# Performance work log

Measured on AMD Instinct MI355X. Metric: run time of the kernel, lower is better.

Reference implementation:

```python
import jax, jax.numpy as jnp
import numpy as np

N_NODES = 100000
N_EDGES = 3200000
IN_DIM = 128


def setup_inputs() -> dict:
    key = jax.random.key(0)
    ks = jax.random.split(key, 6)
    x = jax.random.normal(ks[0], (N_NODES, IN_DIM), dtype=jnp.float32)
    edge_index = jax.random.randint(ks[1], (2, N_EDGES), 0, N_NODES, dtype=jnp.int64)
    # Glorot-ish init for weights, zero bias (PyG GCNConv default has bias)
    W1 = jax.random.normal(ks[2], (IN_DIM, 32), dtype=jnp.float32) / np.sqrt(IN_DIM)
    b1 = jnp.zeros((32,), dtype=jnp.float32)
    W2 = jax.random.normal(ks[3], (32, 16), dtype=jnp.float32) / np.sqrt(32.0)
    b2 = jnp.zeros((16,), dtype=jnp.float32)
    Wf = jax.random.normal(ks[4], (16, 1), dtype=jnp.float32) / np.sqrt(16.0)
    bf = jnp.zeros((1,), dtype=jnp.float32)
    return {"x": x, "edge_index": edge_index, "W1": W1, "b1": b1,
            "W2": W2, "b2": b2, "Wf": Wf, "bf": bf}


def reference(x, edge_index, W1, b1, W2, b2, Wf, bf):
    N = x.shape[0]
    # PyG GCNConv: add self-loops, symmetric normalization D^-1/2 (A+I) D^-1/2
    loop = jnp.arange(N, dtype=edge_index.dtype)
    src = jnp.concatenate([edge_index[0], loop])  # message sources (x_j)
    dst = jnp.concatenate([edge_index[1], loop])  # aggregation targets
    deg = jax.ops.segment_sum(jnp.ones_like(dst, dtype=x.dtype), dst, num_segments=N)
    dinv = jax.lax.rsqrt(jnp.maximum(deg, 1.0))  # deg >= 1 due to self-loops
    norm = dinv[src] * dinv[dst]                  # per-edge coefficient

    def gcn_conv(h, W, b):
        h = h @ W                                 # linear transform first (small dim)
        msg = h[src] * norm[:, None]              # gather + scale
        return jax.ops.segment_sum(msg, dst, num_segments=N) + b  # scatter-add

    h = jax.nn.relu(gcn_conv(x, W1, b1))
    h = jax.nn.relu(gcn_conv(h, W2, b2))
    return (h @ Wf + bf).squeeze(-1)              # [N]
```

## Files before the change

kernel.cpp:

```cpp
#include <hip/hip_runtime.h>


#define TPB 256
#define NBUCK 512
#define BCAP 8192
#define CHUNK 8192

__device__ __forceinline__ unsigned f2bf(float f) {
    unsigned u = __float_as_uint(f);
    return (u + 0x7FFFu + ((u >> 16) & 1u)) >> 16;
}
__device__ __forceinline__ float bflo(unsigned u) { return __uint_as_float(u << 16); }
__device__ __forceinline__ float bfhi(unsigned u) { return __uint_as_float(u & 0xFFFF0000u); }

__global__ __launch_bounds__(512) void binA2_kernel(
        const int* __restrict__ src, const int* __restrict__ dst,
        int* __restrict__ bcur, unsigned* __restrict__ staging, int E, int NPB) {
    __shared__ unsigned packed[CHUNK];
    __shared__ unsigned short buckb[CHUNK];
    __shared__ int hist[NBUCK];
    __shared__ int scan_[NBUCK];
    __shared__ int lstart[NBUCK];
    __shared__ int lcur[NBUCK];
    __shared__ int gbase[NBUCK];
    int tid = threadIdx.x;
    int start = blockIdx.x * CHUNK;
    int sz = min(CHUNK, E - start);

    hist[tid] = 0;
    __syncthreads();
    for (int i = tid; i < sz; i += 512) {
        unsigned d = (unsigned)dst[start + i];
        atomicAdd(&hist[d / (unsigned)NPB], 1);
    }
    __syncthreads();
    int v = hist[tid];
    scan_[tid] = v;
    __syncthreads();
    for (int dd = 1; dd < NBUCK; dd <<= 1) {
        int t = (tid >= dd) ? scan_[tid - dd] : 0;
        __syncthreads();
        scan_[tid] += t;
        __syncthreads();
    }
    lstart[tid] = scan_[tid] - v;
    lcur[tid] = 0;
    gbase[tid] = atomicAdd(&bcur[tid], v);
    __syncthreads();
    for (int i = tid; i < sz; i += 512) {
        unsigned d = (unsigned)dst[start + i];
        unsigned s = (unsigned)src[start + i];
        unsigned b = d / (unsigned)NPB;
        unsigned loc = d - b * (unsigned)NPB;
        int pos = atomicAdd(&lcur[b], 1);
        int si = lstart[b] + pos;
        packed[si] = (loc << 20) | s;
        buckb[si] = (unsigned short)b;
    }
    __syncthreads();
    for (int i = tid; i < sz; i += 512) {
        unsigned b = buckb[i];
        int dsti = gbase[b] + (i - lstart[b]);
        if (dsti < BCAP)
            staging[(size_t)b * BCAP + dsti] = packed[i];
    }
}

__global__ void buildB_kernel(const int* __restrict__ bcur,
                              const unsigned* __restrict__ staging,
                              int* __restrict__ offs, int* __restrict__ counts,
                              float* __restrict__ dinv, int* __restrict__ csr_src,
                              int N, int NPB) {
    __shared__ int sb[NBUCK];
    __shared__ int hist[512];
    __shared__ int scan_[512];
    __shared__ int cur[512];
    int b = blockIdx.x;
    int tid = threadIdx.x;
    if (tid < NBUCK) sb[tid] = min(bcur[tid], BCAP);
    __syncthreads();
    for (int d = 1; d < NBUCK; d <<= 1) {
        int t = 0;
        if (tid < NBUCK && tid >= d) t = sb[tid - d];
        __syncthreads();
        if (tid < NBUCK) sb[tid] += t;
        __syncthreads();
    }
    int sz = min(bcur[b], BCAP);
    int base = (b == 0) ? 0 : sb[b - 1];
    int n0 = b * NPB;
    int nn = min(NPB, N - n0);
    const unsigned* se = staging + (size_t)b * BCAP;

    hist[tid] = 0;
    __syncthreads();
    for (int i = tid; i < sz; i += 512)
        atomicAdd(&hist[se[i] >> 20], 1);
    __syncthreads();
    int h = hist[tid];
    scan_[tid] = h;
    __syncthreads();
    for (int d = 1; d < 512; d <<= 1) {
        int t = (tid >= d) ? scan_[tid - d] : 0;
        __syncthreads();
        scan_[tid] += t;
        __syncthreads();
    }
    int excl = scan_[tid] - h;
    cur[tid] = excl;
    if (tid < nn) {
        int node = n0 + tid;
        offs[node] = base + excl;
        counts[node] = h;
        dinv[node] = rsqrtf((float)(h + 1));
    }
    __syncthreads();
    for (int i = tid; i < sz; i += 512) {
        unsigned p = se[i];
        int pos = atomicAdd(&cur[p >> 20], 1);
        csr_src[base + pos] = (int)(p & 0xFFFFFu);
    }
}

__global__ __launch_bounds__(256) void gemm1_kernel(
        const float* __restrict__ x, const float* __restrict__ W1,
        const float* __restrict__ dinv, unsigned* __restrict__ xwd, int N) {
    __shared__ float ws_[128 * 32];
    for (int i = threadIdx.x; i < 128 * 32; i += 256) ws_[i] = W1[i];
    __syncthreads();
    int t = threadIdx.x;
    int jq = (t & 3) * 8;
    int n0 = blockIdx.x * 256 + (t >> 2) * 4;
    if (n0 >= N) return;
    int nc0 = min(n0 + 0, N - 1);
    int nc1 = min(n0 + 1, N - 1);
    int nc2 = min(n0 + 2, N - 1);
    int nc3 = min(n0 + 3, N - 1);
    const float4* xr0 = (const float4*)(x + (size_t)nc0 * 128);
    const float4* xr1 = (const float4*)(x + (size_t)nc1 * 128);
    const float4* xr2 = (const float4*)(x + (size_t)nc2 * 128);
    const float4* xr3 = (const float4*)(x + (size_t)nc3 * 128);
    float acc[4][8];
#pragma unroll
    for (int n = 0; n < 4; ++n)
#pragma unroll
        for (int j = 0; j < 8; ++j) acc[n][j] = 0.0f;
#pragma unroll 2
    for (int k4 = 0; k4 < 32; ++k4) {
        const float* wb = ws_ + (k4 * 4) * 32 + jq;
        float4 a0 = *(const float4*)(wb);
        float4 a1 = *(const float4*)(wb + 4);
        float4 b0 = *(const float4*)(wb + 32);
        float4 b1v = *(const float4*)(wb + 36);
        float4 c0 = *(const float4*)(wb + 64);
        float4 c1 = *(const float4*)(wb + 68);
        float4 d0 = *(const float4*)(wb + 96);
        float4 d1 = *(const float4*)(wb + 100);
        float4 xv0 = xr0[k4];
        float4 xv1 = xr1[k4];
        float4 xv2 = xr2[k4];
        float4 xv3 = xr3[k4];
#pragma unroll
        for (int n = 0; n < 4; ++n) {
            float4 xv = (n == 0) ? xv0 : (n == 1) ? xv1 : (n == 2) ? xv2 : xv3;
            acc[n][0] += xv.x * a0.x + xv.y * b0.x + xv.z * c0.x + xv.w * d0.x;
            acc[n][1] += xv.x * a0.y + xv.y * b0.y + xv.z * c0.y + xv.w * d0.y;
            acc[n][2] += xv.x * a0.z + xv.y * b0.z + xv.z * c0.z + xv.w * d0.z;
            acc[n][3] += xv.x * a0.w + xv.y * b0.w + xv.z * c0.w + xv.w * d0.w;
            acc[n][4] += xv.x * a1.x + xv.y * b1v.x + xv.z * c1.x + xv.w * d1.x;
            acc[n][5] += xv.x * a1.y + xv.y * b1v.y + xv.z * c1.y + xv.w * d1.y;
            acc[n][6] += xv.x * a1.z + xv.y * b1v.z + xv.z * c1.z + xv.w * d1.z;
            acc[n][7] += xv.x * a1.w + xv.y * b1v.w + xv.z * c1.w + xv.w * d1.w;
        }
    }
#pragma unroll
    for (int n = 0; n < 4; ++n) {
        int node = n0 + n;
        if (node >= N) break;
        float d = dinv[node];
        unsigned pk0 = f2bf(acc[n][0] * d) | (f2bf(acc[n][1] * d) << 16);
        unsigned pk1 = f2bf(acc[n][2] * d) | (f2bf(acc[n][3] * d) << 16);
        unsigned pk2 = f2bf(acc[n][4] * d) | (f2bf(acc[n][5] * d) << 16);
        unsigned pk3 = f2bf(acc[n][6] * d) | (f2bf(acc[n][7] * d) << 16);
        ((uint4*)(xwd + (size_t)node * 16))[t & 3] = make_uint4(pk0, pk1, pk2, pk3);
    }
}

__global__ __launch_bounds__(256) void aggF_kernel(
        const int* __restrict__ offs, const int* __restrict__ counts,
        const int* __restrict__ csr_src, const float* __restrict__ dinv,
        const unsigned* __restrict__ xwd, const float* __restrict__ b1,
        const float* __restrict__ W2, unsigned* __restrict__ h2wd, int N) {
    __shared__ float ws2[32 * 16];
    for (int i = threadIdx.x; i < 512; i += 256) ws2[i] = W2[i];
    __syncthreads();
    int t = threadIdx.x;
    int q = t & 3;
    int node = blockIdx.x * 64 + (t >> 2);
    if (node >= N) return;
    int off = offs[node];
    int deg = counts[node];
    float acc[8];
    {
        uint4 v = ((const uint4*)(xwd + (size_t)node * 16))[q];
        acc[0] = bflo(v.x); acc[1] = bfhi(v.x);
        acc[2] = bflo(v.y); acc[3] = bfhi(v.y);
        acc[4] = bflo(v.z); acc[5] = bfhi(v.z);
        acc[6] = bflo(v.w); acc[7] = bfhi(v.w);
    }
    int i = 0;
    for (; i + 3 < deg; i += 4) {
        int s0 = csr_src[off + i];
        int s1 = csr_src[off + i + 1];
        int s2 = csr_src[off + i + 2];
        int s3 = csr_src[off + i + 3];
        uint4 v0 = ((const uint4*)(xwd + (size_t)s0 * 16))[q];
        uint4 v1 = ((const uint4*)(xwd + (size_t)s1 * 16))[q];
        uint4 v2 = ((const uint4*)(xwd + (size_t)s2 * 16))[q];
        uint4 v3 = ((const uint4*)(xwd + (size_t)s3 * 16))[q];
        acc[0] += (bflo(v0.x) + bflo(v1.x)) + (bflo(v2.x) + bflo(v3.x));
        acc[1] += (bfhi(v0.x) + bfhi(v1.x)) + (bfhi(v2.x) + bfhi(v3.x));
        acc[2] += (bflo(v0.y) + bflo(v1.y)) + (bflo(v2.y) + bflo(v3.y));
        acc[3] += (bfhi(v0.y) + bfhi(v1.y)) + (bfhi(v2.y) + bfhi(v3.y));
        acc[4] += (bflo(v0.z) + bflo(v1.z)) + (bflo(v2.z) + bflo(v3.z));
        acc[5] += (bfhi(v0.z) + bfhi(v1.z)) + (bfhi(v2.z) + bfhi(v3.z));
        acc[6] += (bflo(v0.w) + bflo(v1.w)) + (bflo(v2.w) + bflo(v3.w));
        acc[7] += (bfhi(v0.w) + bfhi(v1.w)) + (bfhi(v2.w) + bfhi(v3.w));
    }
    for (; i < deg; ++i) {
        int s = csr_src[off + i];
        uint4 v = ((const uint4*)(xwd + (size_t)s * 16))[q];
        acc[0] += bflo(v.x); acc[1] += bfhi(v.x);
        acc[2] += bflo(v.y); acc[3] += bfhi(v.y);
        acc[4] += bflo(v.z); acc[5] += bfhi(v.z);
        acc[6] += bflo(v.w); acc[7] += bfhi(v.w);
    }
    float dv = dinv[node];
    float part[16];
#pragma unroll
    for (int j = 0; j < 16; ++j) part[j] = 0.0f;
    const float* bq = b1 + q * 8;
#pragma unroll
    for (int k = 0; k < 8; ++k) {
        float h = fmaxf(acc[k] * dv + bq[k], 0.0f);
        const float* wr = ws2 + (q * 8 + k) * 16;
        float4 w0 = *(const float4*)(wr);
        float4 w1 = *(const float4*)(wr + 4);
        float4 w2 = *(const float4*)(wr + 8);
        float4 w3 = *(const float4*)(wr + 12);
        part[0]  += h * w0.x; part[1]  += h * w0.y; part[2]  += h * w0.z; part[3]  += h * w0.w;
        part[4]  += h * w1.x; part[5]  += h * w1.y; part[6]  += h * w1.z; part[7]  += h * w1.w;
        part[8]  += h * w2.x; part[9]  += h * w2.y; part[10] += h * w2.z; part[11] += h * w2.w;
        part[12] += h * w3.x; part[13] += h * w3.y; part[14] += h * w3.z; part[15] += h * w3.w;
    }
    float p8[8];
#pragma unroll
    for (int j = 0; j < 8; ++j) {
        float send = (q & 1) ? part[j] : part[j + 8];
        float keep = (q & 1) ? part[j + 8] : part[j];
        p8[j] = keep + __shfl_xor(send, 1, 64);
    }
    float p4[4];
#pragma unroll
    for (int j = 0; j < 4; ++j) {
        float send = (q & 2) ? p8[j] : p8[j + 4];
        float keep = (q & 2) ? p8[j + 4] : p8[j];
        p4[j] = keep + __shfl_xor(send, 2, 64);
    }
    unsigned pk0 = f2bf(p4[0] * dv) | (f2bf(p4[1] * dv) << 16);
    unsigned pk1 = f2bf(p4[2] * dv) | (f2bf(p4[3] * dv) << 16);
    int slot = ((q & 1) << 1) | ((q >> 1) & 1);
    ((uint2*)(h2wd + (size_t)node * 8))[slot] = make_uint2(pk0, pk1);
}

__global__ __launch_bounds__(256) void aggS16f_kernel(
        const int* __restrict__ offs, const int* __restrict__ counts,
        const int* __restrict__ csr_src, const float* __restrict__ dinv,
        const unsigned* __restrict__ h2wd,
        const float* __restrict__ b2, const float* __restrict__ Wf,
        const float* __restrict__ bf, float* __restrict__ out, int N) {
    __shared__ float bs_[16];
    __shared__ float wf_[16];
    __shared__ float bfv;
    int t = threadIdx.x;
    if (t < 16) { bs_[t] = b2[t]; wf_[t] = Wf[t]; }
    if (t == 0) bfv = bf[0];
    __syncthreads();
    int q = t & 1;
    int node = blockIdx.x * 128 + (t >> 1);
    if (node >= N) return;
    int off = offs[node];
    int deg = counts[node];
    float acc[8];
    {
        uint4 v = ((const uint4*)(h2wd + (size_t)node * 8))[q];
        acc[0] = bflo(v.x); acc[1] = bfhi(v.x);
        acc[2] = bflo(v.y); acc[3] = bfhi(v.y);
        acc[4] = bflo(v.z); acc[5] = bfhi(v.z);
        acc[6] = bflo(v.w); acc[7] = bfhi(v.w);
    }
    int i = 0;
    for (; i + 3 < deg; i += 4) {
        int s0 = csr_src[off + i];
        int s1 = csr_src[off + i + 1];
        int s2 = csr_src[off + i + 2];
        int s3 = csr_src[off + i + 3];
        uint4 v0 = ((const uint4*)(h2wd + (size_t)s0 * 8))[q];
        uint4 v1 = ((const uint4*)(h2wd + (size_t)s1 * 8))[q];
        uint4 v2 = ((const uint4*)(h2wd + (size_t)s2 * 8))[q];
        uint4 v3 = ((const uint4*)(h2wd + (size_t)s3 * 8))[q];
        acc[0] += (bflo(v0.x) + bflo(v1.x)) + (bflo(v2.x) + bflo(v3.x));
        acc[1] += (bfhi(v0.x) + bfhi(v1.x)) + (bfhi(v2.x) + bfhi(v3.x));
        acc[2] += (bflo(v0.y) + bflo(v1.y)) + (bflo(v2.y) + bflo(v3.y));
        acc[3] += (bfhi(v0.y) + bfhi(v1.y)) + (bfhi(v2.y) + bfhi(v3.y));
        acc[4] += (bflo(v0.z) + bflo(v1.z)) + (bflo(v2.z) + bflo(v3.z));
        acc[5] += (bfhi(v0.z) + bfhi(v1.z)) + (bfhi(v2.z) + bfhi(v3.z));
        acc[6] += (bflo(v0.w) + bflo(v1.w)) + (bflo(v2.w) + bflo(v3.w));
        acc[7] += (bfhi(v0.w) + bfhi(v1.w)) + (bfhi(v2.w) + bfhi(v3.w));
    }
    for (; i < deg; ++i) {
        int s = csr_src[off + i];
        uint4 v = ((const uint4*)(h2wd + (size_t)s * 8))[q];
        acc[0] += bflo(v.x); acc[1] += bfhi(v.x);
        acc[2] += bflo(v.y); acc[3] += bfhi(v.y);
        acc[4] += bflo(v.z); acc[5] += bfhi(v.z);
        acc[6] += bflo(v.w); acc[7] += bfhi(v.w);
    }
    float dv = dinv[node];
    const float* bq = bs_ + q * 8;
    const float* wq = wf_ + q * 8;
    float part = 0.f;
#pragma unroll
    for (int k = 0; k < 8; ++k)
        part += fmaxf(acc[k] * dv + bq[k], 0.f) * wq[k];
    part += __shfl_xor(part, 1, 64);
    if (q == 0) out[node] = part + bfv;
}

extern "C" void kernel_launch(void* const* d_in, const int* in_sizes, int n_in,
                              void* d_out, int out_size, void* d_ws, size_t ws_size,
                              hipStream_t stream) {
    const float* x  = (const float*)d_in[0];
    const int*   ei = (const int*)d_in[1];
    const float* W1 = (const float*)d_in[2];
    const float* b1 = (const float*)d_in[3];
    const float* W2 = (const float*)d_in[4];
    const float* b2 = (const float*)d_in[5];
    const float* Wf = (const float*)d_in[6];
    const float* bf = (const float*)d_in[7];

    int N = in_sizes[0] / 128;
    int E = in_sizes[1] / 2;
    const int* src = ei;
    const int* dst = ei + E;
    int NPB = (N + NBUCK - 1) / NBUCK;

    size_t Np = ((size_t)N + 3) & ~(size_t)3;
    size_t Ep = ((size_t)E + 3) & ~(size_t)3;
    int* wsI      = (int*)d_ws;
    int* counts   = wsI;
    int* offs     = counts + Np;
    int* bcur     = offs + Np;
    int* csr_src  = bcur + NBUCK;
    float* dinv   = (float*)(csr_src + Ep);
    unsigned* xwd = (unsigned*)(dinv + Np);
    unsigned* staging = xwd + 16 * Np;
    unsigned* h2wd = staging;
    float* out    = (float*)d_out;

    int nbG1 = (N + 255) / 256;
    int nbC  = (E + CHUNK - 1) / CHUNK;
    int nbA32 = (N + 63) / 64;
    int nbA16 = (N + 127) / 128;

    hipMemsetAsync(bcur, 0, NBUCK * sizeof(int), stream);
    binA2_kernel<<<nbC, 512, 0, stream>>>(src, dst, bcur, staging, E, NPB);
    buildB_kernel<<<NBUCK, 512, 0, stream>>>(bcur, staging, offs, counts,
                                             dinv, csr_src, N, NPB);
    gemm1_kernel<<<nbG1, 256, 0, stream>>>(x, W1, dinv, xwd, N);
    aggF_kernel<<<nbA32, 256, 0, stream>>>(offs, counts, csr_src, dinv, xwd,
                                           b1, W2, h2wd, N);
    aggS16f_kernel<<<nbA16, 256, 0, stream>>>(offs, counts, csr_src, dinv, h2wd,
                                              b2, Wf, bf, out, N);
}
```

Before: 253.3 us.

## Use wave-shuffle scans, register-staged binning, split bucket base scan, smaller GEMM tiles

Replaces the shared-memory Hillis-Steele scans with a wave-shuffle exclusive scan, and halves CHUNK so the binning kernel runs more blocks. The binning kernels now keep edge data in registers instead of reading global memory twice. The per-block redundant 512-entry bucket scan in buildB moves into a separate single-block kernel, and gemm1 handles 2 nodes per thread instead of 4 for more blocks. In exchange it adds one kernel launch and raises register pressure; buildB's 16-register staging assumes bucket size stays within BCAP.

```diff
diff --git a/kernel.cpp b/kernel.cpp
--- a/kernel.cpp
+++ b/kernel.cpp
@@ -4,7 +4,7 @@
 #define TPB 256
 #define NBUCK 512
 #define BCAP 8192
-#define CHUNK 8192
+#define CHUNK 4096
 
 __device__ __forceinline__ unsigned f2bf(float f) {
     unsigned u = __float_as_uint(f);
@@ -12,6 +12,30 @@
 }
 __device__ __forceinline__ float bflo(unsigned u) { return __uint_as_float(u << 16); }
 __device__ __forceinline__ float bfhi(unsigned u) { return __uint_as_float(u & 0xFFFF0000u); }
+
+__device__ __forceinline__ int excl_scan_512(int v, int* wsum, int tid) {
+    int lane = tid & 63, wv = tid >> 6;
+    int x = v;
+#pragma unroll
+    for (int d = 1; d < 64; d <<= 1) {
+        int y = __shfl_up(x, d, 64);
+        if (lane >= d) x += y;
+    }
+    if (lane == 63) wsum[wv] = x;
+    __syncthreads();
+    if (tid < 64) {
+        int s = (lane < 8) ? wsum[lane] : 0;
+#pragma unroll
+        for (int d = 1; d < 8; d <<= 1) {
+            int y = __shfl_up(s, d, 64);
+            if (lane >= d) s += y;
+        }
+        if (lane < 8) wsum[lane] = s;
+    }
+    __syncthreads();
+    int base = (wv > 0) ? wsum[wv - 1] : 0;
+    return base + x - v;
+}
 
 __global__ __launch_bounds__(512) void binA2_kernel(
         const int* __restrict__ src, const int* __restrict__ dst,
@@ -19,42 +43,46 @@
     __shared__ unsigned packed[CHUNK];
     __shared__ unsigned short buckb[CHUNK];
     __shared__ int hist[NBUCK];
-    __shared__ int scan_[NBUCK];
     __shared__ int lstart[NBUCK];
     __shared__ int lcur[NBUCK];
     __shared__ int gbase[NBUCK];
+    __shared__ int wsum[8];
     int tid = threadIdx.x;
     int start = blockIdx.x * CHUNK;
     int sz = min(CHUNK, E - start);
 
+    unsigned dreg[8], sreg[8];
     hist[tid] = 0;
-    __syncthreads();
-    for (int i = tid; i < sz; i += 512) {
-        unsigned d = (unsigned)dst[start + i];
-        atomicAdd(&hist[d / (unsigned)NPB], 1);
-    }
+#pragma unroll
+    for (int c = 0; c < 8; ++c) {
+        int i = tid + c * 512;
+        if (i < sz) {
+            dreg[c] = (unsigned)dst[start + i];
+            sreg[c] = (unsigned)src[start + i];
+        } else {
+            dreg[c] = 0xFFFFFFFFu;
+        }
+    }
+    __syncthreads();
+#pragma unroll
+    for (int c = 0; c < 8; ++c)
+        if (dreg[c] != 0xFFFFFFFFu) atomicAdd(&hist[dreg[c] / (unsigned)NPB], 1);
     __syncthreads();
     int v = hist[tid];
-    scan_[tid] = v;
-    __syncthreads();
-    for (int dd = 1; dd < NBUCK; dd <<= 1) {
-        int t = (tid >= dd) ? scan_[tid - dd] : 0;
-        __syncthreads();
-        scan_[tid] += t;
-        __syncthreads();
-    }
-    lstart[tid] = scan_[tid] - v;
+    int excl = excl_scan_512(v, wsum, tid);
+    lstart[tid] = excl;
     lcur[tid] = 0;
     gbase[tid] = atomicAdd(&bcur[tid], v);
     __syncthreads();
-    for (int i = tid; i < sz; i += 512) {
-        unsigned d = (unsigned)dst[start + i];
-        unsigned s = (unsigned)src[start + i];
+#pragma unroll
+    for (int c = 0; c < 8; ++c) {
+        if (dreg[c] == 0xFFFFFFFFu) continue;
+        unsigned d = dreg[c];
         unsigned b = d / (unsigned)NPB;
         unsigned loc = d - b * (unsigned)NPB;
         int pos = atomicAdd(&lcur[b], 1);
         int si = lstart[b] + pos;
-        packed[si] = (loc << 20) | s;
+        packed[si] = (loc << 20) | sreg[c];
         buckb[si] = (unsigned short)b;
     }
     __syncthreads();
@@ -66,47 +94,45 @@
     }
 }
 
-__global__ void buildB_kernel(const int* __restrict__ bcur,
-                              const unsigned* __restrict__ staging,
-                              int* __restrict__ offs, int* __restrict__ counts,
-                              float* __restrict__ dinv, int* __restrict__ csr_src,
-                              int N, int NPB) {
-    __shared__ int sb[NBUCK];
+__global__ __launch_bounds__(512) void bbase_kernel(
+        const int* __restrict__ bcur, int* __restrict__ bbase) {
+    __shared__ int wsum[8];
+    int tid = threadIdx.x;
+    int v = min(bcur[tid], BCAP);
+    bbase[tid] = excl_scan_512(v, wsum, tid);
+}
+
+__global__ __launch_bounds__(512) void buildB_kernel(
+        const int* __restrict__ bcur, const int* __restrict__ bbase,
+        const unsigned* __restrict__ staging,
+        int* __restrict__ offs, int* __restrict__ counts,
+        float* __restrict__ dinv, int* __restrict__ csr_src,
+        int N, int NPB) {
     __shared__ int hist[512];
-    __shared__ int scan_[512];
     __shared__ int cur[512];
+    __shared__ int wsum[8];
     int b = blockIdx.x;
     int tid = threadIdx.x;
-    if (tid < NBUCK) sb[tid] = min(bcur[tid], BCAP);
-    __syncthreads();
-    for (int d = 1; d < NBUCK; d <<= 1) {
-        int t = 0;
-        if (tid < NBUCK && tid >= d) t = sb[tid - d];
-        __syncthreads();
-        if (tid < NBUCK) sb[tid] += t;
-        __syncthreads();
-    }
     int sz = min(bcur[b], BCAP);
-    int base = (b == 0) ? 0 : sb[b - 1];
+    int base = bbase[b];
     int n0 = b * NPB;
     int nn = min(NPB, N - n0);
     const unsigned* se = staging + (size_t)b * BCAP;
 
+    unsigned preg[16];
     hist[tid] = 0;
-    __syncthreads();
-    for (int i = tid; i < sz; i += 512)
-        atomicAdd(&hist[se[i] >> 20], 1);
+#pragma unroll
+    for (int c = 0; c < 16; ++c) {
+        int i = tid + c * 512;
+        preg[c] = (i < sz) ? se[i] : 0xFFFFFFFFu;
+    }
+    __syncthreads();
+#pragma unroll
+    for (int c = 0; c < 16; ++c)
+        if (preg[c] != 0xFFFFFFFFu) atomicAdd(&hist[preg[c] >> 20], 1);
     __syncthreads();
     int h = hist[tid];
-    scan_[tid] = h;
-    __syncthreads();
-    for (int d = 1; d < 512; d <<= 1) {
-        int t = (tid >= d) ? scan_[tid - d] : 0;
-        __syncthreads();
-        scan_[tid] += t;
-        __syncthreads();
-    }
-    int excl = scan_[tid] - h;
+    int excl = excl_scan_512(h, wsum, tid);
     cur[tid] = excl;
     if (tid < nn) {
         int node = n0 + tid;
@@ -115,8 +141,10 @@
         dinv[node] = rsqrtf((float)(h + 1));
     }
     __syncthreads();
-    for (int i = tid; i < sz; i += 512) {
-        unsigned p = se[i];
+#pragma unroll
+    for (int c = 0; c < 16; ++c) {
+        unsigned p = preg[c];
+        if (p == 0xFFFFFFFFu) continue;
         int pos = atomicAdd(&cur[p >> 20], 1);
         csr_src[base + pos] = (int)(p & 0xFFFFFu);
     }
@@ -130,19 +158,15 @@
     __syncthreads();
     int t = threadIdx.x;
     int jq = (t & 3) * 8;
-    int n0 = blockIdx.x * 256 + (t >> 2) * 4;
+    int n0 = blockIdx.x * 128 + (t >> 2) * 2;
     if (n0 >= N) return;
     int nc0 = min(n0 + 0, N - 1);
     int nc1 = min(n0 + 1, N - 1);
-    int nc2 = min(n0 + 2, N - 1);
-    int nc3 = min(n0 + 3, N - 1);
     const float4* xr0 = (const float4*)(x + (size_t)nc0 * 128);
     const float4* xr1 = (const float4*)(x + (size_t)nc1 * 128);
-    const float4* xr2 = (const float4*)(x + (size_t)nc2 * 128);
-    const float4* xr3 = (const float4*)(x + (size_t)nc3 * 128);
-    float acc[4][8];
-#pragma unroll
-    for (int n = 0; n < 4; ++n)
+    float acc[2][8];
+#pragma unroll
+    for (int n = 0; n < 2; ++n)
 #pragma unroll
         for (int j = 0; j < 8; ++j) acc[n][j] = 0.0f;
 #pragma unroll 2
@@ -158,11 +182,9 @@
         float4 d1 = *(const float4*)(wb + 100);
         float4 xv0 = xr0[k4];
         float4 xv1 = xr1[k4];
-        float4 xv2 = xr2[k4];
-        float4 xv3 = xr3[k4];
-#pragma unroll
-        for (int n = 0; n < 4; ++n) {
-            float4 xv = (n == 0) ? xv0 : (n == 1) ? xv1 : (n == 2) ? xv2 : xv3;
+#pragma unroll
+        for (int n = 0; n < 2; ++n) {
+            float4 xv = (n == 0) ? xv0 : xv1;
             acc[n][0] += xv.x * a0.x + xv.y * b0.x + xv.z * c0.x + xv.w * d0.x;
             acc[n][1] += xv.x * a0.y + xv.y * b0.y + xv.z * c0.y + xv.w * d0.y;
             acc[n][2] += xv.x * a0.z + xv.y * b0.z + xv.z * c0.z + xv.w * d0.z;
@@ -174,7 +196,7 @@
         }
     }
 #pragma unroll
-    for (int n = 0; n < 4; ++n) {
+    for (int n = 0; n < 2; ++n) {
         int node = n0 + n;
         if (node >= N) break;
         float d = dinv[node];
@@ -361,21 +383,23 @@
     int* counts   = wsI;
     int* offs     = counts + Np;
     int* bcur     = offs + Np;
-    int* csr_src  = bcur + NBUCK;
+    int* bbase    = bcur + NBUCK;
+    int* csr_src  = bbase + NBUCK;
     float* dinv   = (float*)(csr_src + Ep);
     unsigned* xwd = (unsigned*)(dinv + Np);
     unsigned* staging = xwd + 16 * Np;
     unsigned* h2wd = staging;
     float* out    = (float*)d_out;
 
-    int nbG1 = (N + 255) / 256;
     int nbC  = (E + CHUNK - 1) / CHUNK;
+    int nbG1 = (N + 127) / 128;
     int nbA32 = (N + 63) / 64;
     int nbA16 = (N + 127) / 128;
 
     hipMemsetAsync(bcur, 0, NBUCK * sizeof(int), stream);
     binA2_kernel<<<nbC, 512, 0, stream>>>(src, dst, bcur, staging, E, NPB);
-    buildB_kernel<<<NBUCK, 512, 0, stream>>>(bcur, staging, offs, counts,
+    bbase_kernel<<<1, 512, 0, stream>>>(bcur, bbase);
+    buildB_kernel<<<NBUCK, 512, 0, stream>>>(bcur, bbase, staging, offs, counts,
                                              dinv, csr_src, N, NPB);
     gemm1_kernel<<<nbG1, 256, 0, stream>>>(x, W1, dinv, xwd, N);
     aggF_kernel<<<nbA32, 256, 0, stream>>>(offs, counts, csr_src, dinv, xwd,
```

Result: no change. 251.2 us (-0.8%).
